# Optimization experiments

Hardware: AMD Instinct MI355X
Metric: run time of the kernel (lower is better)

The kernel has to match this reference:

```python
import jax, jax.numpy as jnp
import numpy as np

B, S, D, H = 2, 2048, 1024, 16
HD = D // H
NEG_INF = jnp.finfo(jnp.float32).min


def setup_inputs() -> dict:
    key = jax.random.key(0)
    ks = jax.random.split(key, 6)
    s = 1.0 / np.sqrt(D)
    return {
        'x': jax.random.normal(ks[0], (B, S, D), dtype=jnp.float32),
        'Wq': jax.random.normal(ks[1], (D, D), dtype=jnp.float32) * s,
        'Wk': jax.random.normal(ks[2], (D, D), dtype=jnp.float32) * s,
        'Wv': jax.random.normal(ks[3], (D, D), dtype=jnp.float32) * s,
        'Wo': jax.random.normal(ks[4], (D, D), dtype=jnp.float32) * s,
        'bo': jnp.zeros((D,), dtype=jnp.float32),
    }


def reference(x, Wq, Wk, Wv, Wo, bo):
    b, s, _ = x.shape
    scale = HD ** -0.5
    # Q/K/V projections: einsum('bnd,di->bni') == x @ W
    def proj(W):
        return jnp.einsum('bnd,di->bni', x, W).reshape(b, s, H, HD).transpose(0, 2, 1, 3)
    Q, K, V = proj(Wq), proj(Wk), proj(Wv)  # [b,h,s,hd]
    scores = jnp.einsum('bhnd,bhmd->bhnm', Q, K) * scale  # [b,h,s,s]
    causal = jnp.tril(jnp.ones((s, s), dtype=bool))
    scores = jnp.where(causal[None, None], scores, NEG_INF)
    attn = jax.nn.softmax(scores, axis=-1)
    ctx = jnp.einsum('bhnm,bhmd->bhnd', attn, V)
    ctx = ctx.transpose(0, 2, 1, 3).reshape(b, s, D)
    # nn.Linear: ctx @ Wo.T + bo
    return jnp.einsum('bnd,od->bno', ctx, Wo) + bo
```

## Files before the change

kernel.cpp:

```cpp
#include <hip/hip_runtime.h>

#define B_  2
#define S_  2048
#define D_  1024
#define H_  16
#define HD_ 64
#define M_  (B_*S_)

typedef __attribute__((ext_vector_type(8))) short s16x8;
typedef __attribute__((ext_vector_type(4))) float f32x4;
typedef __attribute__((ext_vector_type(16))) float f32x16;

__device__ __forceinline__ unsigned short f2bf(float f) {
  unsigned int u = __builtin_bit_cast(unsigned int, f);
  u += 0x7fffu + ((u >> 16) & 1u);
  return (unsigned short)(u >> 16);
}
__device__ __forceinline__ float bf2f(unsigned short h) {
  unsigned int u = ((unsigned int)h) << 16;
  return __builtin_bit_cast(float, u);
}

__device__ __forceinline__ void gload_lds16(const unsigned short* g, unsigned short* l) {
  __builtin_amdgcn_global_load_lds((const __attribute__((address_space(1))) void*)g,
                                   (__attribute__((address_space(3))) void*)l, 16, 0, 0);
}

__global__ void cvt_kernel(const float* __restrict__ in, unsigned short* __restrict__ out, int n4) {
  int i = blockIdx.x * blockDim.x + threadIdx.x;
  if (i >= n4) return;
  float4 v = reinterpret_cast<const float4*>(in)[i];
  ushort4 o;
  o.x = f2bf(v.x); o.y = f2bf(v.y); o.z = f2bf(v.z); o.w = f2bf(v.w);
  reinterpret_cast<ushort4*>(out)[i] = o;
}

__global__ void transpose_cvt3(const float* __restrict__ W0, const float* __restrict__ W1,
                               const float* __restrict__ W2, unsigned short* __restrict__ dstBase) {
  __shared__ float tile[32][33];
  const float* in = blockIdx.z == 0 ? W0 : (blockIdx.z == 1 ? W1 : W2);
  unsigned short* out = dstBase + (size_t)blockIdx.z * 1024 * 1024;
  const int bx = blockIdx.x, by = blockIdx.y, tx = threadIdx.x;
  const int x = bx * 32 + tx;
  for (int j = threadIdx.y; j < 32; j += 8)
    tile[j][tx] = in[(by * 32 + j) * 1024 + x];
  __syncthreads();
  const int xo = by * 32 + tx;
  for (int j = threadIdx.y; j < 32; j += 8)
    out[(bx * 32 + j) * 1024 + xo] = f2bf(tile[tx][j]);
}

#define BM 128
#define BN 128
#define BK 64

__global__ __launch_bounds__(256, 4) void gemm_bt(
    const unsigned short* __restrict__ A,
    const unsigned short* __restrict__ Bt,
    void* __restrict__ out0, void* __restrict__ out1, void* __restrict__ out2,
    const float* __restrict__ bias,
    const int mode, const float qscale)
{
  __shared__ unsigned short As[BM * BK];
  __shared__ unsigned short Bs[BN * BK];

  const int t    = threadIdx.x;
  const int lane = t & 63;
  const int wid  = t >> 6;
  const int l15  = lane & 15;
  const int g    = lane >> 4;
  const int wm   = wid >> 1;
  const int wn   = wid & 1;

  const int n0 = blockIdx.x * BN;
  const int m0 = blockIdx.y * BM;

  const int lrow = lane >> 3;
  const int lcol = ((lane & 7) ^ lrow) * 8;
  const int rsw  = l15 & 7;

  f32x4 acc[4][4];
#pragma unroll
  for (int i = 0; i < 4; ++i)
#pragma unroll
    for (int j = 0; j < 4; ++j)
      acc[i][j] = (f32x4){0.f, 0.f, 0.f, 0.f};

  for (int kt = 0; kt < 1024 / BK; ++kt) {
    const int k0 = kt * BK;
#pragma unroll
    for (int p = 0; p < 4; ++p) {
      const int c = p * 4 + wid;
      const int row = c * 8 + lrow;
      gload_lds16(&A[(size_t)(m0 + row) * 1024 + k0 + lcol], &As[c * 512]);
      gload_lds16(&Bt[(size_t)(n0 + row) * 1024 + k0 + lcol], &Bs[c * 512]);
    }
    __syncthreads();

#pragma unroll
    for (int kk = 0; kk < 2; ++kk) {
      s16x8 af[4], bf[4];
#pragma unroll
      for (int mi = 0; mi < 4; ++mi)
        af[mi] = *reinterpret_cast<const s16x8*>(
            &As[(wm * 64 + mi * 16 + l15) * BK + (((4 * kk + g) ^ rsw) * 8)]);
#pragma unroll
      for (int ni = 0; ni < 4; ++ni)
        bf[ni] = *reinterpret_cast<const s16x8*>(
            &Bs[(wn * 64 + ni * 16 + l15) * BK + (((4 * kk + g) ^ rsw) * 8)]);
#pragma unroll
      for (int mi = 0; mi < 4; ++mi)
#pragma unroll
        for (int ni = 0; ni < 4; ++ni)
          acc[mi][ni] = __builtin_amdgcn_mfma_f32_16x16x32_bf16(af[mi], bf[ni], acc[mi][ni], 0, 0, 0);
    }
    __syncthreads();
  }

  if (mode == 0) {
    const int sel = n0 >> 10;
    const int nl0 = n0 & 1023;
    if (sel < 2) {
      unsigned short* outb = (unsigned short*)(sel == 0 ? out0 : out1);
      const float sc = (sel == 0) ? qscale : 1.0f;
#pragma unroll
      for (int mi = 0; mi < 4; ++mi) {
#pragma unroll
        for (int ni = 0; ni < 4; ++ni) {
          const int n = nl0 + wn * 64 + ni * 16 + l15;
          const int h = n >> 6, hd = n & 63;
#pragma unroll
          for (int r = 0; r < 4; ++r) {
            const int m = m0 + wm * 64 + mi * 16 + 4 * g + r;
            const int b = m >> 11, s = m & 2047;
            outb[(((b * H_ + h) * S_) + s) * HD_ + hd] = f2bf(acc[mi][ni][r] * sc);
          }
        }
      }
    } else {
      unsigned short* outb = (unsigned short*)out2;
#pragma unroll
      for (int mi = 0; mi < 4; ++mi) {
#pragma unroll
        for (int ni = 0; ni < 4; ++ni) {
          const int n = nl0 + wn * 64 + ni * 16 + l15;
          const int h = n >> 6, hd = n & 63;
          const int m = m0 + wm * 64 + mi * 16 + 4 * g;
          const int b = m >> 11, s = m & 2047;
          ushort4 o;
          o.x = f2bf(acc[mi][ni][0]);
          o.y = f2bf(acc[mi][ni][1]);
          o.z = f2bf(acc[mi][ni][2]);
          o.w = f2bf(acc[mi][ni][3]);
          *reinterpret_cast<ushort4*>(&outb[(((b * H_ + h) * HD_) + hd) * S_ + s]) = o;
        }
      }
    }
  } else {
    float* outf = (float*)out0;
#pragma unroll
    for (int mi = 0; mi < 4; ++mi) {
#pragma unroll
      for (int ni = 0; ni < 4; ++ni) {
        const int n = n0 + wn * 64 + ni * 16 + l15;
        const float bv = bias[n];
#pragma unroll
        for (int r = 0; r < 4; ++r) {
          const int m = m0 + wm * 64 + mi * 16 + 4 * g + r;
          outf[m * 1024 + n] = acc[mi][ni][r] + bv;
        }
      }
    }
  }
}

__global__ __launch_bounds__(256) void attn_kernel(
    const unsigned short* __restrict__ Q,
    const unsigned short* __restrict__ K,
    const unsigned short* __restrict__ VT,
    unsigned short* __restrict__ Ctx,
    unsigned short* __restrict__ pctx,
    float* __restrict__ pml)
{
  __shared__ unsigned short Kl[2][64 * 64];
  __shared__ unsigned short Vl[2][64 * 64];
  __shared__ unsigned short Pl[4][2][32][40];

  static const unsigned char QBv[24] = {15,15,7,14,14,13,13,6,12,12,11,11,5,10,10,9,9,4,8,8,3,2,1,0};
  static const signed char   HFv[24] = {0,1,-1,0,1,0,1,-1,0,1,0,1,-1,0,1,0,1,-1,0,1,-1,-1,-1,-1};

  const int t    = threadIdx.x;
  const int lane = t & 63;
  const int w    = t >> 6;
  const int q    = lane & 31;
  const int hi   = lane >> 5;

  const int bh = blockIdx.x;
  const int qb = QBv[blockIdx.y];
  const int hf = HFv[blockIdx.y];
  const long base  = (long)bh * S_ * HD_;
  const long vbase = (long)bh * HD_ * S_;
  const int q0w = qb * 128 + w * 32;

  int ktBeg, ktEnd;
  if (hf < 0) { ktBeg = 0; ktEnd = 2 * qb + 2; }
  else        { ktBeg = hf * (qb + 1); ktEnd = ktBeg + qb + 1; }

  const int srow = lane >> 3;
  const int scol = ((lane & 7) ^ srow) * 8;
  const int swz  = (q & 7) * 8;

  s16x8 qf[4];
#pragma unroll
  for (int s = 0; s < 4; ++s)
    qf[s] = *reinterpret_cast<const s16x8*>(&Q[base + (long)(q0w + q) * HD_ + 16 * s + 8 * hi]);

  f32x16 ctx0, ctx1;
#pragma unroll
  for (int r = 0; r < 16; ++r) { ctx0[r] = 0.f; ctx1[r] = 0.f; }
  float m_run = -1e30f, l_run = 0.f;

#pragma unroll
  for (int p = 0; p < 2; ++p) {
    const int c = 2 * w + p;
    gload_lds16(&K[base + (long)(ktBeg * 64 + c * 8 + srow) * HD_ + scol], &Kl[0][c * 512]);
    gload_lds16(&VT[vbase + (long)(c * 8 + srow) * S_ + ktBeg * 64 + scol], &Vl[0][c * 512]);
  }
  __syncthreads();

  for (int kt = ktBeg; kt < ktEnd; ++kt) {
    const int cur  = (kt - ktBeg) & 1;
    const int kv64 = kt * 64;

    if (kt + 1 < ktEnd) {
      const int nk = (kt + 1) * 64;
#pragma unroll
      for (int p = 0; p < 2; ++p) {
        const int c = 2 * w + p;
        gload_lds16(&K[base + (long)(nk + c * 8 + srow) * HD_ + scol], &Kl[cur ^ 1][c * 512]);
        gload_lds16(&VT[vbase + (long)(c * 8 + srow) * S_ + nk + scol], &Vl[cur ^ 1][c * 512]);
      }
    }

    if (kv64 <= q0w + 31) {
      f32x16 sa0, sa1;
#pragma unroll
      for (int r = 0; r < 16; ++r) { sa0[r] = 0.f; sa1[r] = 0.f; }
      __builtin_amdgcn_s_setprio(1);
#pragma unroll
      for (int s = 0; s < 4; ++s) {
        const s16x8 kb0 = *reinterpret_cast<const s16x8*>(&Kl[cur][(q) * 64 + ((16 * s + 8 * hi) ^ swz)]);
        sa0 = __builtin_amdgcn_mfma_f32_32x32x16_bf16(kb0, qf[s], sa0, 0, 0, 0);
      }
#pragma unroll
      for (int s = 0; s < 4; ++s) {
        const s16x8 kb1 = *reinterpret_cast<const s16x8*>(&Kl[cur][(32 + q) * 64 + ((16 * s + 8 * hi) ^ swz)]);
        sa1 = __builtin_amdgcn_mfma_f32_32x32x16_bf16(kb1, qf[s], sa1, 0, 0, 0);
      }
      __builtin_amdgcn_s_setprio(0);

      if (kv64 + 64 > q0w) {
#pragma unroll
        for (int r = 0; r < 16; ++r) {
          const int kl = (r & 3) + 8 * (r >> 2) + 4 * hi;
          if (kv64 + kl > q0w + q)      sa0[r] = -1e30f;
          if (kv64 + 32 + kl > q0w + q) sa1[r] = -1e30f;
        }
      }

      float mx;
      {
        float a0 = fmaxf(fmaxf(sa0[0], sa0[1]), fmaxf(sa0[2], sa0[3]));
        float a1 = fmaxf(fmaxf(sa0[4], sa0[5]), fmaxf(sa0[6], sa0[7]));
        float a2 = fmaxf(fmaxf(sa0[8], sa0[9]), fmaxf(sa0[10], sa0[11]));
        float a3 = fmaxf(fmaxf(sa0[12], sa0[13]), fmaxf(sa0[14], sa0[15]));
        float b0 = fmaxf(fmaxf(sa1[0], sa1[1]), fmaxf(sa1[2], sa1[3]));
        float b1 = fmaxf(fmaxf(sa1[4], sa1[5]), fmaxf(sa1[6], sa1[7]));
        float b2 = fmaxf(fmaxf(sa1[8], sa1[9]), fmaxf(sa1[10], sa1[11]));
        float b3 = fmaxf(fmaxf(sa1[12], sa1[13]), fmaxf(sa1[14], sa1[15]));
        mx = fmaxf(fmaxf(fmaxf(a0, a1), fmaxf(a2, a3)), fmaxf(fmaxf(b0, b1), fmaxf(b2, b3)));
        mx = fmaxf(mx, __shfl_xor(mx, 32));
      }
      if (mx > m_run + 8.f) {
        const float alpha = __builtin_amdgcn_exp2f(m_run - mx);
        m_run = mx;
        l_run *= alpha;
#pragma unroll
        for (int r = 0; r < 16; ++r) { ctx0[r] *= alpha; ctx1[r] *= alpha; }
      }

      float p0[16], p1[16];
#pragma unroll
      for (int r = 0; r < 16; ++r) {
        p0[r] = __builtin_amdgcn_exp2f(sa0[r] - m_run);
        p1[r] = __builtin_amdgcn_exp2f(sa1[r] - m_run);
      }
      float ps;
      {
        float s0 = ((p0[0] + p0[1]) + (p0[2] + p0[3])) + ((p0[4] + p0[5]) + (p0[6] + p0[7]));
        float s1 = ((p0[8] + p0[9]) + (p0[10] + p0[11])) + ((p0[12] + p0[13]) + (p0[14] + p0[15]));
        float s2 = ((p1[0] + p1[1]) + (p1[2] + p1[3])) + ((p1[4] + p1[5]) + (p1[6] + p1[7]));
        float s3 = ((p1[8] + p1[9]) + (p1[10] + p1[11])) + ((p1[12] + p1[13]) + (p1[14] + p1[15]));
        ps = (s0 + s1) + (s2 + s3);
        ps += __shfl_xor(ps, 32);
      }
      l_run += ps;

#pragma unroll
      for (int c = 0; c < 4; ++c) {
        unsigned int pk01, pk23;
        asm("v_cvt_pk_bf16_f32 %0, %1, %2" : "=v"(pk01) : "v"(p0[4 * c + 0]), "v"(p0[4 * c + 1]));
        asm("v_cvt_pk_bf16_f32 %0, %1, %2" : "=v"(pk23) : "v"(p0[4 * c + 2]), "v"(p0[4 * c + 3]));
        uint2 pr; pr.x = pk01; pr.y = pk23;
        *reinterpret_cast<uint2*>(&Pl[w][0][q][8 * c + 4 * hi]) = pr;
      }
#pragma unroll
      for (int c = 0; c < 4; ++c) {
        unsigned int pk01, pk23;
        asm("v_cvt_pk_bf16_f32 %0, %1, %2" : "=v"(pk01) : "v"(p1[4 * c + 0]), "v"(p1[4 * c + 1]));
        asm("v_cvt_pk_bf16_f32 %0, %1, %2" : "=v"(pk23) : "v"(p1[4 * c + 2]), "v"(p1[4 * c + 3]));
        uint2 pr; pr.x = pk01; pr.y = pk23;
        *reinterpret_cast<uint2*>(&Pl[w][1][q][8 * c + 4 * hi]) = pr;
      }

      __builtin_amdgcn_s_setprio(1);
#pragma unroll
      for (int kc = 0; kc < 4; ++kc) {
        const s16x8 pf = *reinterpret_cast<const s16x8*>(&Pl[w][kc >> 1][q][16 * (kc & 1) + 8 * hi]);
        const s16x8 v0 = *reinterpret_cast<const s16x8*>(&Vl[cur][(q) * 64 + ((16 * kc + 8 * hi) ^ swz)]);
        ctx0 = __builtin_amdgcn_mfma_f32_32x32x16_bf16(v0, pf, ctx0, 0, 0, 0);
        const s16x8 v1 = *reinterpret_cast<const s16x8*>(&Vl[cur][(32 + q) * 64 + ((16 * kc + 8 * hi) ^ swz)]);
        ctx1 = __builtin_amdgcn_mfma_f32_32x32x16_bf16(v1, pf, ctx1, 0, 0, 0);
      }
      __builtin_amdgcn_s_setprio(0);
    }

    __syncthreads();
  }

  if (hf < 0) {
    const int b = bh >> 4, h = bh & 15;
    const float inv = 1.f / l_run;
    unsigned short* orow = &Ctx[((long)b * S_ + q0w + q) * D_ + h * 64];
#pragma unroll
    for (int c = 0; c < 4; ++c) {
      ushort4 o0, o1;
      o0.x = f2bf(ctx0[4 * c] * inv);     o0.y = f2bf(ctx0[4 * c + 1] * inv);
      o0.z = f2bf(ctx0[4 * c + 2] * inv); o0.w = f2bf(ctx0[4 * c + 3] * inv);
      o1.x = f2bf(ctx1[4 * c] * inv);     o1.y = f2bf(ctx1[4 * c + 1] * inv);
      o1.z = f2bf(ctx1[4 * c + 2] * inv); o1.w = f2bf(ctx1[4 * c + 3] * inv);
      *reinterpret_cast<ushort4*>(&orow[8 * c + 4 * hi])      = o0;
      *reinterpret_cast<ushort4*>(&orow[32 + 8 * c + 4 * hi]) = o1;
    }
  } else {
    const int sidx = ((bh << 3) + (qb - 8)) * 2 + hf;
    const int rloc = w * 32 + q;
    unsigned short* prow = &pctx[((long)sidx * 128 + rloc) * 64];
#pragma unroll
    for (int c = 0; c < 4; ++c) {
      ushort4 o0, o1;
      o0.x = f2bf(ctx0[4 * c]);     o0.y = f2bf(ctx0[4 * c + 1]);
      o0.z = f2bf(ctx0[4 * c + 2]); o0.w = f2bf(ctx0[4 * c + 3]);
      o1.x = f2bf(ctx1[4 * c]);     o1.y = f2bf(ctx1[4 * c + 1]);
      o1.z = f2bf(ctx1[4 * c + 2]); o1.w = f2bf(ctx1[4 * c + 3]);
      *reinterpret_cast<ushort4*>(&prow[8 * c + 4 * hi])      = o0;
      *reinterpret_cast<ushort4*>(&prow[32 + 8 * c + 4 * hi]) = o1;
    }
    if (hi == 0) {
      pml[((long)sidx * 128 + rloc) * 2]     = m_run;
      pml[((long)sidx * 128 + rloc) * 2 + 1] = l_run;
    }
  }
}

__global__ __launch_bounds__(256) void merge_kernel(
    const unsigned short* __restrict__ pctx,
    const float* __restrict__ pml,
    unsigned short* __restrict__ Ctx)
{
  const int unit = blockIdx.x;
  const int bh = unit >> 3;
  const int qb = (unit & 7) + 8;
  const long s0 = (long)unit * 2, s1 = s0 + 1;

  const int t   = threadIdx.x;
  const int row = t >> 1;
  const int hh  = t & 1;

  const long r0 = s0 * 128 + row;
  const long r1 = s1 * 128 + row;
  const float m0 = pml[r0 * 2], l0 = pml[r0 * 2 + 1];
  const float m1 = pml[r1 * 2], l1 = pml[r1 * 2 + 1];
  const float M  = fmaxf(m0, m1);
  const float a0 = __builtin_amdgcn_exp2f(m0 - M);
  const float a1 = __builtin_amdgcn_exp2f(m1 - M);
  const float inv = 1.f / (l0 * a0 + l1 * a1);

  const unsigned short* c0p = &pctx[r0 * 64 + hh * 32];
  const unsigned short* c1p = &pctx[r1 * 64 + hh * 32];
  const int b = bh >> 4, h = bh & 15;
  unsigned short* op = &Ctx[((long)b * S_ + qb * 128 + row) * D_ + h * 64 + hh * 32];

#pragma unroll
  for (int j = 0; j < 32; j += 8) {
    const s16x8 v0 = *reinterpret_cast<const s16x8*>(&c0p[j]);
    const s16x8 v1 = *reinterpret_cast<const s16x8*>(&c1p[j]);
    s16x8 o;
#pragma unroll
    for (int e = 0; e < 8; ++e) {
      const float f = (bf2f((unsigned short)v0[e]) * a0 + bf2f((unsigned short)v1[e]) * a1) * inv;
      o[e] = (short)f2bf(f);
    }
    *reinterpret_cast<s16x8*>(&op[j]) = o;
  }
}

extern "C" void kernel_launch(void* const* d_in, const int* in_sizes, int n_in,
                              void* d_out, int out_size, void* d_ws, size_t ws_size,
                              hipStream_t stream) {
  const float* x  = (const float*)d_in[0];
  const float* Wq = (const float*)d_in[1];
  const float* Wk = (const float*)d_in[2];
  const float* Wv = (const float*)d_in[3];
  const float* Wo = (const float*)d_in[4];
  const float* bo = (const float*)d_in[5];
  float* out = (float*)d_out;

  char* ws = (char*)d_ws;
  const size_t MB = 1024 * 1024;
  unsigned short* xb  = (unsigned short*)(ws + 0 * MB);
  unsigned short* WT  = (unsigned short*)(ws + 8 * MB);
  unsigned short* Wob = (unsigned short*)(ws + 14 * MB);
  unsigned short* Qb  = (unsigned short*)(ws + 16 * MB);
  unsigned short* Kb  = (unsigned short*)(ws + 24 * MB);
  unsigned short* VTb = (unsigned short*)(ws + 32 * MB);
  unsigned short* Cx  = (unsigned short*)(ws + 40 * MB);
  unsigned short* pctx = (unsigned short*)(ws + 0 * MB);
  float*          pml  = (float*)(ws + 8 * MB);

  cvt_kernel<<<(M_ * D_ / 4 + 255) / 256, 256, 0, stream>>>(x, xb, M_ * D_ / 4);
  cvt_kernel<<<(D_ * D_ / 4 + 255) / 256, 256, 0, stream>>>(Wo, Wob, D_ * D_ / 4);
  transpose_cvt3<<<dim3(32, 32, 3), dim3(32, 8), 0, stream>>>(Wq, Wk, Wv, WT);

  gemm_bt<<<dim3(3 * D_ / BN, M_ / BM), 256, 0, stream>>>(
      xb, WT, (void*)Qb, (void*)Kb, (void*)VTb, nullptr, 0, 0.18033688011112042f);

  attn_kernel<<<dim3(B_ * H_, 24), 256, 0, stream>>>(Qb, Kb, VTb, Cx, pctx, pml);
  merge_kernel<<<256, 256, 0, stream>>>(pctx, pml, Cx);

  gemm_bt<<<dim3(D_ / BN, M_ / BM), 256, 0, stream>>>(
      Cx, Wob, (void*)out, nullptr, nullptr, bo, 1, 1.0f);
}
```

Measured before the change: 116.4 us.

## Rebalance causal attention work with multi-segment splits and paired small q-blocks

```diff
diff --git a/kernel.cpp b/kernel.cpp
--- a/kernel.cpp
+++ b/kernel.cpp
@@ -20,6 +20,9 @@
   unsigned int u = ((unsigned int)h) << 16;
   return __builtin_bit_cast(float, u);
 }
+
+__device__ __forceinline__ float xhalf_max(float v) { return fmaxf(v, __shfl_xor(v, 32)); }
+__device__ __forceinline__ float xhalf_sum(float v) { return v + __shfl_xor(v, 32); }
 
 __device__ __forceinline__ void gload_lds16(const unsigned short* g, unsigned short* l) {
   __builtin_amdgcn_global_load_lds((const __attribute__((address_space(1))) void*)g,
@@ -186,8 +189,11 @@
   __shared__ unsigned short Vl[2][64 * 64];
   __shared__ unsigned short Pl[4][2][32][40];
 
-  static const unsigned char QBv[24] = {15,15,7,14,14,13,13,6,12,12,11,11,5,10,10,9,9,4,8,8,3,2,1,0};
-  static const signed char   HFv[24] = {0,1,-1,0,1,0,1,-1,0,1,0,1,-1,0,1,0,1,-1,0,1,-1,-1,-1,-1};
+  static const signed char QB0v[24] = {15,15,15,14,14,14,13,13,12,12,11,11,10,10, 9, 9, 8, 8, 7, 7, 6, 5, 4, 3};
+  static const signed char BG0v[24] = { 0,11,22, 0,10,20, 0,14, 0,13, 0,12, 0,11, 0,10, 0, 9, 0, 8, 0, 0, 0, 0};
+  static const signed char EN0v[24] = {11,22,32,10,20,30,14,28,13,26,12,24,11,22,10,20, 9,18, 8,16,14,12,10, 8};
+  static const signed char SL0v[24] = {17,18,19,14,15,16,12,13,10,11, 8, 9, 6, 7, 4, 5, 2, 3, 0, 1,-1,-1,-1,-1};
+  static const signed char QB1v[24] = {-1,-1,-1,-1,-1,-1,-1,-1,-1,-1,-1,-1,-1,-1,-1,-1,-1,-1,-1,-1,-1, 0, 1, 2};
 
   const int t    = threadIdx.x;
   const int lane = t & 63;
@@ -196,179 +202,182 @@
   const int hi   = lane >> 5;
 
   const int bh = blockIdx.x;
-  const int qb = QBv[blockIdx.y];
-  const int hf = HFv[blockIdx.y];
+  const int y  = blockIdx.y;
   const long base  = (long)bh * S_ * HD_;
   const long vbase = (long)bh * HD_ * S_;
-  const int q0w = qb * 128 + w * 32;
-
-  int ktBeg, ktEnd;
-  if (hf < 0) { ktBeg = 0; ktEnd = 2 * qb + 2; }
-  else        { ktBeg = hf * (qb + 1); ktEnd = ktBeg + qb + 1; }
 
   const int srow = lane >> 3;
   const int scol = ((lane & 7) ^ srow) * 8;
   const int swz  = (q & 7) * 8;
-
-  s16x8 qf[4];
-#pragma unroll
-  for (int s = 0; s < 4; ++s)
-    qf[s] = *reinterpret_cast<const s16x8*>(&Q[base + (long)(q0w + q) * HD_ + 16 * s + 8 * hi]);
-
-  f32x16 ctx0, ctx1;
-#pragma unroll
-  for (int r = 0; r < 16; ++r) { ctx0[r] = 0.f; ctx1[r] = 0.f; }
-  float m_run = -1e30f, l_run = 0.f;
-
-#pragma unroll
-  for (int p = 0; p < 2; ++p) {
-    const int c = 2 * w + p;
-    gload_lds16(&K[base + (long)(ktBeg * 64 + c * 8 + srow) * HD_ + scol], &Kl[0][c * 512]);
-    gload_lds16(&VT[vbase + (long)(c * 8 + srow) * S_ + ktBeg * 64 + scol], &Vl[0][c * 512]);
-  }
-  __syncthreads();
-
-  for (int kt = ktBeg; kt < ktEnd; ++kt) {
-    const int cur  = (kt - ktBeg) & 1;
-    const int kv64 = kt * 64;
-
-    if (kt + 1 < ktEnd) {
-      const int nk = (kt + 1) * 64;
-#pragma unroll
-      for (int p = 0; p < 2; ++p) {
-        const int c = 2 * w + p;
-        gload_lds16(&K[base + (long)(nk + c * 8 + srow) * HD_ + scol], &Kl[cur ^ 1][c * 512]);
-        gload_lds16(&VT[vbase + (long)(c * 8 + srow) * S_ + nk + scol], &Vl[cur ^ 1][c * 512]);
-      }
-    }
-
-    if (kv64 <= q0w + 31) {
-      f32x16 sa0, sa1;
-#pragma unroll
-      for (int r = 0; r < 16; ++r) { sa0[r] = 0.f; sa1[r] = 0.f; }
-      __builtin_amdgcn_s_setprio(1);
-#pragma unroll
-      for (int s = 0; s < 4; ++s) {
-        const s16x8 kb0 = *reinterpret_cast<const s16x8*>(&Kl[cur][(q) * 64 + ((16 * s + 8 * hi) ^ swz)]);
-        sa0 = __builtin_amdgcn_mfma_f32_32x32x16_bf16(kb0, qf[s], sa0, 0, 0, 0);
-      }
-#pragma unroll
-      for (int s = 0; s < 4; ++s) {
-        const s16x8 kb1 = *reinterpret_cast<const s16x8*>(&Kl[cur][(32 + q) * 64 + ((16 * s + 8 * hi) ^ swz)]);
-        sa1 = __builtin_amdgcn_mfma_f32_32x32x16_bf16(kb1, qf[s], sa1, 0, 0, 0);
-      }
-      __builtin_amdgcn_s_setprio(0);
-
-      if (kv64 + 64 > q0w) {
+  const int pkey = q >> 3;
+
+  for (int ps = 0; ps < 2; ++ps) {
+    int qb, ktBeg, ktEnd, slot;
+    if (ps == 0) { qb = QB0v[y]; ktBeg = BG0v[y]; ktEnd = EN0v[y]; slot = SL0v[y]; }
+    else         { qb = QB1v[y]; if (qb < 0) break; ktBeg = 0; ktEnd = 2 * qb + 2; slot = -1; }
+
+    const int q0w = qb * 128 + w * 32;
+
+    s16x8 qf[4];
+#pragma unroll
+    for (int s = 0; s < 4; ++s)
+      qf[s] = *reinterpret_cast<const s16x8*>(&Q[base + (long)(q0w + q) * HD_ + 16 * s + 8 * hi]);
+
+    f32x16 ctx0, ctx1;
+#pragma unroll
+    for (int r = 0; r < 16; ++r) { ctx0[r] = 0.f; ctx1[r] = 0.f; }
+    float m_run = -1e30f, l_run = 0.f;
+
+#pragma unroll
+    for (int p = 0; p < 2; ++p) {
+      const int c = 2 * w + p;
+      gload_lds16(&K[base + (long)(ktBeg * 64 + c * 8 + srow) * HD_ + scol], &Kl[0][c * 512]);
+      gload_lds16(&VT[vbase + (long)(c * 8 + srow) * S_ + ktBeg * 64 + scol], &Vl[0][c * 512]);
+    }
+    __syncthreads();
+
+    for (int kt = ktBeg; kt < ktEnd; ++kt) {
+      const int cur  = (kt - ktBeg) & 1;
+      const int kv64 = kt * 64;
+
+      if (kt + 1 < ktEnd) {
+        const int nk = (kt + 1) * 64;
+#pragma unroll
+        for (int p = 0; p < 2; ++p) {
+          const int c = 2 * w + p;
+          gload_lds16(&K[base + (long)(nk + c * 8 + srow) * HD_ + scol], &Kl[cur ^ 1][c * 512]);
+          gload_lds16(&VT[vbase + (long)(c * 8 + srow) * S_ + nk + scol], &Vl[cur ^ 1][c * 512]);
+        }
+      }
+
+      if (kv64 <= q0w + 31) {
+        f32x16 sa0, sa1;
+#pragma unroll
+        for (int r = 0; r < 16; ++r) { sa0[r] = 0.f; sa1[r] = 0.f; }
+        __builtin_amdgcn_s_setprio(1);
+#pragma unroll
+        for (int s = 0; s < 4; ++s) {
+          const s16x8 kb0 = *reinterpret_cast<const s16x8*>(&Kl[cur][(q) * 64 + ((16 * s + 8 * hi) ^ swz)]);
+          sa0 = __builtin_amdgcn_mfma_f32_32x32x16_bf16(kb0, qf[s], sa0, 0, 0, 0);
+        }
+#pragma unroll
+        for (int s = 0; s < 4; ++s) {
+          const s16x8 kb1 = *reinterpret_cast<const s16x8*>(&Kl[cur][(32 + q) * 64 + ((16 * s + 8 * hi) ^ swz)]);
+          sa1 = __builtin_amdgcn_mfma_f32_32x32x16_bf16(kb1, qf[s], sa1, 0, 0, 0);
+        }
+        __builtin_amdgcn_s_setprio(0);
+
+        if (kv64 + 64 > q0w) {
+#pragma unroll
+          for (int r = 0; r < 16; ++r) {
+            const int kl = (r & 3) + 8 * (r >> 2) + 4 * hi;
+            if (kv64 + kl > q0w + q)      sa0[r] = -1e30f;
+            if (kv64 + 32 + kl > q0w + q) sa1[r] = -1e30f;
+          }
+        }
+
+        float mx;
+        {
+          float a0 = fmaxf(fmaxf(sa0[0], sa0[1]), fmaxf(sa0[2], sa0[3]));
+          float a1 = fmaxf(fmaxf(sa0[4], sa0[5]), fmaxf(sa0[6], sa0[7]));
+          float a2 = fmaxf(fmaxf(sa0[8], sa0[9]), fmaxf(sa0[10], sa0[11]));
+          float a3 = fmaxf(fmaxf(sa0[12], sa0[13]), fmaxf(sa0[14], sa0[15]));
+          float b0 = fmaxf(fmaxf(sa1[0], sa1[1]), fmaxf(sa1[2], sa1[3]));
+          float b1 = fmaxf(fmaxf(sa1[4], sa1[5]), fmaxf(sa1[6], sa1[7]));
+          float b2 = fmaxf(fmaxf(sa1[8], sa1[9]), fmaxf(sa1[10], sa1[11]));
+          float b3 = fmaxf(fmaxf(sa1[12], sa1[13]), fmaxf(sa1[14], sa1[15]));
+          mx = fmaxf(fmaxf(fmaxf(a0, a1), fmaxf(a2, a3)), fmaxf(fmaxf(b0, b1), fmaxf(b2, b3)));
+          mx = xhalf_max(mx);
+        }
+        if (mx > m_run + 8.f) {
+          const float alpha = __builtin_amdgcn_exp2f(m_run - mx);
+          m_run = mx;
+          l_run *= alpha;
+#pragma unroll
+          for (int r = 0; r < 16; ++r) { ctx0[r] *= alpha; ctx1[r] *= alpha; }
+        }
+
+        float p0[16], p1[16];
 #pragma unroll
         for (int r = 0; r < 16; ++r) {
-          const int kl = (r & 3) + 8 * (r >> 2) + 4 * hi;
-          if (kv64 + kl > q0w + q)      sa0[r] = -1e30f;
-          if (kv64 + 32 + kl > q0w + q) sa1[r] = -1e30f;
-        }
-      }
-
-      float mx;
-      {
-        float a0 = fmaxf(fmaxf(sa0[0], sa0[1]), fmaxf(sa0[2], sa0[3]));
-        float a1 = fmaxf(fmaxf(sa0[4], sa0[5]), fmaxf(sa0[6], sa0[7]));
-        float a2 = fmaxf(fmaxf(sa0[8], sa0[9]), fmaxf(sa0[10], sa0[11]));
-        float a3 = fmaxf(fmaxf(sa0[12], sa0[13]), fmaxf(sa0[14], sa0[15]));
-        float b0 = fmaxf(fmaxf(sa1[0], sa1[1]), fmaxf(sa1[2], sa1[3]));
-        float b1 = fmaxf(fmaxf(sa1[4], sa1[5]), fmaxf(sa1[6], sa1[7]));
-        float b2 = fmaxf(fmaxf(sa1[8], sa1[9]), fmaxf(sa1[10], sa1[11]));
-        float b3 = fmaxf(fmaxf(sa1[12], sa1[13]), fmaxf(sa1[14], sa1[15]));
-        mx = fmaxf(fmaxf(fmaxf(a0, a1), fmaxf(a2, a3)), fmaxf(fmaxf(b0, b1), fmaxf(b2, b3)));
-        mx = fmaxf(mx, __shfl_xor(mx, 32));
-      }
-      if (mx > m_run + 8.f) {
-        const float alpha = __builtin_amdgcn_exp2f(m_run - mx);
-        m_run = mx;
-        l_run *= alpha;
-#pragma unroll
-        for (int r = 0; r < 16; ++r) { ctx0[r] *= alpha; ctx1[r] *= alpha; }
-      }
-
-      float p0[16], p1[16];
-#pragma unroll
-      for (int r = 0; r < 16; ++r) {
-        p0[r] = __builtin_amdgcn_exp2f(sa0[r] - m_run);
-        p1[r] = __builtin_amdgcn_exp2f(sa1[r] - m_run);
-      }
-      float ps;
-      {
-        float s0 = ((p0[0] + p0[1]) + (p0[2] + p0[3])) + ((p0[4] + p0[5]) + (p0[6] + p0[7]));
-        float s1 = ((p0[8] + p0[9]) + (p0[10] + p0[11])) + ((p0[12] + p0[13]) + (p0[14] + p0[15]));
-        float s2 = ((p1[0] + p1[1]) + (p1[2] + p1[3])) + ((p1[4] + p1[5]) + (p1[6] + p1[7]));
-        float s3 = ((p1[8] + p1[9]) + (p1[10] + p1[11])) + ((p1[12] + p1[13]) + (p1[14] + p1[15]));
-        ps = (s0 + s1) + (s2 + s3);
-        ps += __shfl_xor(ps, 32);
-      }
-      l_run += ps;
-
+          p0[r] = __builtin_amdgcn_exp2f(sa0[r] - m_run);
+          p1[r] = __builtin_amdgcn_exp2f(sa1[r] - m_run);
+        }
+        float psum;
+        {
+          float s0 = ((p0[0] + p0[1]) + (p0[2] + p0[3])) + ((p0[4] + p0[5]) + (p0[6] + p0[7]));
+          float s1 = ((p0[8] + p0[9]) + (p0[10] + p0[11])) + ((p0[12] + p0[13]) + (p0[14] + p0[15]));
+          float s2 = ((p1[0] + p1[1]) + (p1[2] + p1[3])) + ((p1[4] + p1[5]) + (p1[6] + p1[7]));
+          float s3 = ((p1[8] + p1[9]) + (p1[10] + p1[11])) + ((p1[12] + p1[13]) + (p1[14] + p1[15]));
+          psum = xhalf_sum((s0 + s1) + (s2 + s3));
+        }
+        l_run += psum;
+
+#pragma unroll
+        for (int c = 0; c < 4; ++c) {
+          unsigned int pk01, pk23;
+          asm("v_cvt_pk_bf16_f32 %0, %1, %2" : "=v"(pk01) : "v"(p0[4 * c + 0]), "v"(p0[4 * c + 1]));
+          asm("v_cvt_pk_bf16_f32 %0, %1, %2" : "=v"(pk23) : "v"(p0[4 * c + 2]), "v"(p0[4 * c + 3]));
+          uint2 pr; pr.x = pk01; pr.y = pk23;
+          *reinterpret_cast<uint2*>(&Pl[w][0][q][((c ^ pkey) * 8) + 4 * hi]) = pr;
+        }
+#pragma unroll
+        for (int c = 0; c < 4; ++c) {
+          unsigned int pk01, pk23;
+          asm("v_cvt_pk_bf16_f32 %0, %1, %2" : "=v"(pk01) : "v"(p1[4 * c + 0]), "v"(p1[4 * c + 1]));
+          asm("v_cvt_pk_bf16_f32 %0, %1, %2" : "=v"(pk23) : "v"(p1[4 * c + 2]), "v"(p1[4 * c + 3]));
+          uint2 pr; pr.x = pk01; pr.y = pk23;
+          *reinterpret_cast<uint2*>(&Pl[w][1][q][((c ^ pkey) * 8) + 4 * hi]) = pr;
+        }
+
+        __builtin_amdgcn_s_setprio(1);
+#pragma unroll
+        for (int kc = 0; kc < 4; ++kc) {
+          const s16x8 pf = *reinterpret_cast<const s16x8*>(
+              &Pl[w][kc >> 1][q][((2 * (kc & 1) + hi) ^ pkey) * 8]);
+          const s16x8 v0 = *reinterpret_cast<const s16x8*>(&Vl[cur][(q) * 64 + ((16 * kc + 8 * hi) ^ swz)]);
+          ctx0 = __builtin_amdgcn_mfma_f32_32x32x16_bf16(v0, pf, ctx0, 0, 0, 0);
+          const s16x8 v1 = *reinterpret_cast<const s16x8*>(&Vl[cur][(32 + q) * 64 + ((16 * kc + 8 * hi) ^ swz)]);
+          ctx1 = __builtin_amdgcn_mfma_f32_32x32x16_bf16(v1, pf, ctx1, 0, 0, 0);
+        }
+        __builtin_amdgcn_s_setprio(0);
+      }
+
+      __syncthreads();
+    }
+
+    if (slot < 0) {
+      const int b = bh >> 4, h = bh & 15;
+      const float inv = 1.f / l_run;
+      unsigned short* orow = &Ctx[((long)b * S_ + q0w + q) * D_ + h * 64];
 #pragma unroll
       for (int c = 0; c < 4; ++c) {
-        unsigned int pk01, pk23;
-        asm("v_cvt_pk_bf16_f32 %0, %1, %2" : "=v"(pk01) : "v"(p0[4 * c + 0]), "v"(p0[4 * c + 1]));
-        asm("v_cvt_pk_bf16_f32 %0, %1, %2" : "=v"(pk23) : "v"(p0[4 * c + 2]), "v"(p0[4 * c + 3]));
-        uint2 pr; pr.x = pk01; pr.y = pk23;
-        *reinterpret_cast<uint2*>(&Pl[w][0][q][8 * c + 4 * hi]) = pr;
-      }
+        ushort4 o0, o1;
+        o0.x = f2bf(ctx0[4 * c] * inv);     o0.y = f2bf(ctx0[4 * c + 1] * inv);
+        o0.z = f2bf(ctx0[4 * c + 2] * inv); o0.w = f2bf(ctx0[4 * c + 3] * inv);
+        o1.x = f2bf(ctx1[4 * c] * inv);     o1.y = f2bf(ctx1[4 * c + 1] * inv);
+        o1.z = f2bf(ctx1[4 * c + 2] * inv); o1.w = f2bf(ctx1[4 * c + 3] * inv);
+        *reinterpret_cast<ushort4*>(&orow[8 * c + 4 * hi])      = o0;
+        *reinterpret_cast<ushort4*>(&orow[32 + 8 * c + 4 * hi]) = o1;
+      }
+    } else {
+      const long sidx = (long)bh * 20 + slot;
+      const int rloc = w * 32 + q;
+      unsigned short* prow = &pctx[(sidx * 128 + rloc) * 64];
 #pragma unroll
       for (int c = 0; c < 4; ++c) {
-        unsigned int pk01, pk23;
-        asm("v_cvt_pk_bf16_f32 %0, %1, %2" : "=v"(pk01) : "v"(p1[4 * c + 0]), "v"(p1[4 * c + 1]));
-        asm("v_cvt_pk_bf16_f32 %0, %1, %2" : "=v"(pk23) : "v"(p1[4 * c + 2]), "v"(p1[4 * c + 3]));
-        uint2 pr; pr.x = pk01; pr.y = pk23;
-        *reinterpret_cast<uint2*>(&Pl[w][1][q][8 * c + 4 * hi]) = pr;
-      }
-
-      __builtin_amdgcn_s_setprio(1);
-#pragma unroll
-      for (int kc = 0; kc < 4; ++kc) {
-        const s16x8 pf = *reinterpret_cast<const s16x8*>(&Pl[w][kc >> 1][q][16 * (kc & 1) + 8 * hi]);
-        const s16x8 v0 = *reinterpret_cast<const s16x8*>(&Vl[cur][(q) * 64 + ((16 * kc + 8 * hi) ^ swz)]);
-        ctx0 = __builtin_amdgcn_mfma_f32_32x32x16_bf16(v0, pf, ctx0, 0, 0, 0);
-        const s16x8 v1 = *reinterpret_cast<const s16x8*>(&Vl[cur][(32 + q) * 64 + ((16 * kc + 8 * hi) ^ swz)]);
-        ctx1 = __builtin_amdgcn_mfma_f32_32x32x16_bf16(v1, pf, ctx1, 0, 0, 0);
-      }
-      __builtin_amdgcn_s_setprio(0);
-    }
-
-    __syncthreads();
-  }
-
-  if (hf < 0) {
-    const int b = bh >> 4, h = bh & 15;
-    const float inv = 1.f / l_run;
-    unsigned short* orow = &Ctx[((long)b * S_ + q0w + q) * D_ + h * 64];
-#pragma unroll
-    for (int c = 0; c < 4; ++c) {
-      ushort4 o0, o1;
-      o0.x = f2bf(ctx0[4 * c] * inv);     o0.y = f2bf(ctx0[4 * c + 1] * inv);
-      o0.z = f2bf(ctx0[4 * c + 2] * inv); o0.w = f2bf(ctx0[4 * c + 3] * inv);
-      o1.x = f2bf(ctx1[4 * c] * inv);     o1.y = f2bf(ctx1[4 * c + 1] * inv);
-      o1.z = f2bf(ctx1[4 * c + 2] * inv); o1.w = f2bf(ctx1[4 * c + 3] * inv);
-      *reinterpret_cast<ushort4*>(&orow[8 * c + 4 * hi])      = o0;
-      *reinterpret_cast<ushort4*>(&orow[32 + 8 * c + 4 * hi]) = o1;
-    }
-  } else {
-    const int sidx = ((bh << 3) + (qb - 8)) * 2 + hf;
-    const int rloc = w * 32 + q;
-    unsigned short* prow = &pctx[((long)sidx * 128 + rloc) * 64];
-#pragma unroll
-    for (int c = 0; c < 4; ++c) {
-      ushort4 o0, o1;
-      o0.x = f2bf(ctx0[4 * c]);     o0.y = f2bf(ctx0[4 * c + 1]);
-      o0.z = f2bf(ctx0[4 * c + 2]); o0.w = f2bf(ctx0[4 * c + 3]);
-      o1.x = f2bf(ctx1[4 * c]);     o1.y = f2bf(ctx1[4 * c + 1]);
-      o1.z = f2bf(ctx1[4 * c + 2]); o1.w = f2bf(ctx1[4 * c + 3]);
-      *reinterpret_cast<ushort4*>(&prow[8 * c + 4 * hi])      = o0;
-      *reinterpret_cast<ushort4*>(&prow[32 + 8 * c + 4 * hi]) = o1;
-    }
-    if (hi == 0) {
-      pml[((long)sidx * 128 + rloc) * 2]     = m_run;
-      pml[((long)sidx * 128 + rloc) * 2 + 1] = l_run;
+        ushort4 o0, o1;
+        o0.x = f2bf(ctx0[4 * c]);     o0.y = f2bf(ctx0[4 * c + 1]);
+        o0.z = f2bf(ctx0[4 * c + 2]); o0.w = f2bf(ctx0[4 * c + 3]);
+        o1.x = f2bf(ctx1[4 * c]);     o1.y = f2bf(ctx1[4 * c + 1]);
+        o1.z = f2bf(ctx1[4 * c + 2]); o1.w = f2bf(ctx1[4 * c + 3]);
+        *reinterpret_cast<ushort4*>(&prow[8 * c + 4 * hi])      = o0;
+        *reinterpret_cast<ushort4*>(&prow[32 + 8 * c + 4 * hi]) = o1;
+      }
+      if (hi == 0) {
+        pml[(sidx * 128 + rloc) * 2]     = m_run;
+        pml[(sidx * 128 + rloc) * 2 + 1] = l_run;
+      }
     }
   }
 }
@@ -378,26 +387,33 @@
     const float* __restrict__ pml,
     unsigned short* __restrict__ Ctx)
 {
+  static const signed char slotBase[9] = {0, 2, 4, 6, 8, 10, 12, 14, 17};
+  static const signed char nsegT[9]    = {2, 2, 2, 2, 2, 2, 2, 3, 3};
+
   const int unit = blockIdx.x;
-  const int bh = unit >> 3;
-  const int qb = (unit & 7) + 8;
-  const long s0 = (long)unit * 2, s1 = s0 + 1;
+  const int bh = unit / 9;
+  const int qi = unit % 9;
+  const int qb = 7 + qi;
+  const int ns = nsegT[qi];
+  const long sb = (long)bh * 20 + slotBase[qi];
 
   const int t   = threadIdx.x;
   const int row = t >> 1;
   const int hh  = t & 1;
 
-  const long r0 = s0 * 128 + row;
-  const long r1 = s1 * 128 + row;
-  const float m0 = pml[r0 * 2], l0 = pml[r0 * 2 + 1];
-  const float m1 = pml[r1 * 2], l1 = pml[r1 * 2 + 1];
-  const float M  = fmaxf(m0, m1);
+  float m0 = pml[((sb + 0) * 128 + row) * 2],     l0 = pml[((sb + 0) * 128 + row) * 2 + 1];
+  float m1 = pml[((sb + 1) * 128 + row) * 2],     l1 = pml[((sb + 1) * 128 + row) * 2 + 1];
+  float m2 = -1e30f, l2 = 0.f;
+  if (ns == 3) { m2 = pml[((sb + 2) * 128 + row) * 2]; l2 = pml[((sb + 2) * 128 + row) * 2 + 1]; }
+  const float M  = fmaxf(fmaxf(m0, m1), m2);
   const float a0 = __builtin_amdgcn_exp2f(m0 - M);
   const float a1 = __builtin_amdgcn_exp2f(m1 - M);
-  const float inv = 1.f / (l0 * a0 + l1 * a1);
-
-  const unsigned short* c0p = &pctx[r0 * 64 + hh * 32];
-  const unsigned short* c1p = &pctx[r1 * 64 + hh * 32];
+  const float a2 = (ns == 3) ? __builtin_amdgcn_exp2f(m2 - M) : 0.f;
+  const float inv = 1.f / (l0 * a0 + l1 * a1 + l2 * a2);
+
+  const unsigned short* c0p = &pctx[((sb + 0) * 128 + row) * 64 + hh * 32];
+  const unsigned short* c1p = &pctx[((sb + 1) * 128 + row) * 64 + hh * 32];
+  const unsigned short* c2p = &pctx[((sb + 2) * 128 + row) * 64 + hh * 32];
   const int b = bh >> 4, h = bh & 15;
   unsigned short* op = &Ctx[((long)b * S_ + qb * 128 + row) * D_ + h * 64 + hh * 32];
 
@@ -405,11 +421,14 @@
   for (int j = 0; j < 32; j += 8) {
     const s16x8 v0 = *reinterpret_cast<const s16x8*>(&c0p[j]);
     const s16x8 v1 = *reinterpret_cast<const s16x8*>(&c1p[j]);
+    s16x8 v2;
+    if (ns == 3) v2 = *reinterpret_cast<const s16x8*>(&c2p[j]);
     s16x8 o;
 #pragma unroll
     for (int e = 0; e < 8; ++e) {
-      const float f = (bf2f((unsigned short)v0[e]) * a0 + bf2f((unsigned short)v1[e]) * a1) * inv;
-      o[e] = (short)f2bf(f);
+      float f = bf2f((unsigned short)v0[e]) * a0 + bf2f((unsigned short)v1[e]) * a1;
+      if (ns == 3) f += bf2f((unsigned short)v2[e]) * a2;
+      o[e] = (short)f2bf(f * inv);
     }
     *reinterpret_cast<s16x8*>(&op[j]) = o;
   }
@@ -436,7 +455,7 @@
   unsigned short* VTb = (unsigned short*)(ws + 32 * MB);
   unsigned short* Cx  = (unsigned short*)(ws + 40 * MB);
   unsigned short* pctx = (unsigned short*)(ws + 0 * MB);
-  float*          pml  = (float*)(ws + 8 * MB);
+  float*          pml  = (float*)(ws + 11 * MB);
 
   cvt_kernel<<<(M_ * D_ / 4 + 255) / 256, 256, 0, stream>>>(x, xb, M_ * D_ / 4);
   cvt_kernel<<<(D_ * D_ / 4 + 255) / 256, 256, 0, stream>>>(Wo, Wob, D_ * D_ / 4);
@@ -446,7 +465,7 @@
       xb, WT, (void*)Qb, (void*)Kb, (void*)VTb, nullptr, 0, 0.18033688011112042f);
 
   attn_kernel<<<dim3(B_ * H_, 24), 256, 0, stream>>>(Qb, Kb, VTb, Cx, pctx, pml);
-  merge_kernel<<<256, 256, 0, stream>>>(pctx, pml, Cx);
+  merge_kernel<<<288, 256, 0, stream>>>(pctx, pml, Cx);
 
   gemm_bt<<<dim3(D_ / BN, M_ / BM), 256, 0, stream>>>(
       Cx, Wob, (void*)out, nullptr, nullptr, bo, 1, 1.0f);
```

Measured after the change: 124.9 us. 1.07x slower.
